# Optimization experiments

Hardware: AMD Instinct MI355X
Metric: run time of the kernel (lower is better)

## Reference

```python
import jax, jax.numpy as jnp
import numpy as np

D_MODEL = 1024
NUM_HEADS = 16
HEAD_DIM = D_MODEL // NUM_HEADS
B, S = 4, 2048


def setup_inputs() -> dict:
    key = jax.random.key(0)
    ks = jax.random.split(key, 11)
    scale = 1.0 / np.sqrt(D_MODEL)
    return {
        "query": jax.random.normal(ks[0], (B, S, D_MODEL), dtype=jnp.float32),
        "key": jax.random.normal(ks[1], (B, S, D_MODEL), dtype=jnp.float32),
        "value": jax.random.normal(ks[2], (B, S, D_MODEL), dtype=jnp.float32),
        "Wq": jax.random.normal(ks[3], (D_MODEL, D_MODEL), dtype=jnp.float32) * scale,
        "bq": jnp.zeros((D_MODEL,), dtype=jnp.float32),
        "Wk": jax.random.normal(ks[4], (D_MODEL, D_MODEL), dtype=jnp.float32) * scale,
        "bk": jnp.zeros((D_MODEL,), dtype=jnp.float32),
        "Wv": jax.random.normal(ks[5], (D_MODEL, D_MODEL), dtype=jnp.float32) * scale,
        "bv": jnp.zeros((D_MODEL,), dtype=jnp.float32),
        "Wo": jax.random.normal(ks[6], (D_MODEL, D_MODEL), dtype=jnp.float32) * scale,
        "bo": jnp.zeros((D_MODEL,), dtype=jnp.float32),
    }


def reference(query, key, value, Wq, bq, Wk, bk, Wv, bv, Wo, bo):
    b = query.shape[0]
    # QKV projections, split into heads: [B, H, S, hd]
    Q = (query @ Wq + bq).reshape(b, -1, NUM_HEADS, HEAD_DIM).transpose(0, 2, 1, 3)
    K = (key @ Wk + bk).reshape(b, -1, NUM_HEADS, HEAD_DIM).transpose(0, 2, 1, 3)
    V = (value @ Wv + bv).reshape(b, -1, NUM_HEADS, HEAD_DIM).transpose(0, 2, 1, 3)
    # scaled dot-product attention, full [B, H, S, S] scores (as in original)
    scores = jnp.einsum("bhqd,bhkd->bhqk", Q, K) / jnp.sqrt(
        jnp.asarray(HEAD_DIM, dtype=jnp.float32))
    attn = jax.nn.softmax(scores, axis=-1)
    out = jnp.einsum("bhqk,bhkd->bhqd", attn, V)
    out = out.transpose(0, 2, 1, 3).reshape(b, -1, D_MODEL)
    return out @ Wo + bo
```

## Files before the change

kernel.cpp:

```cpp
#include <hip/hip_runtime.h>
#include <hip/hip_bf16.h>

typedef _Float16 f16;
typedef _Float16 f16x8 __attribute__((ext_vector_type(8)));
typedef _Float16 f16x4 __attribute__((ext_vector_type(4)));
typedef __fp16 h16x2 __attribute__((ext_vector_type(2)));
typedef float f32x4 __attribute__((ext_vector_type(4)));

#define D_MODEL 1024
#define NHEAD 16
#define HD 64
#define BATCH 4
#define SEQ 2048
#define TOK (BATCH * SEQ)

__device__ __forceinline__ void gload_lds16(const void* g, void* l) {
  __builtin_amdgcn_global_load_lds(
      (const __attribute__((address_space(1))) unsigned int*)g,
      (__attribute__((address_space(3))) unsigned int*)l, 16, 0, 0);
}

__device__ __forceinline__ f16x8 fragF16_64(const char* rowptr, int g, int c) {
  union { uint4 u; f16x8 v; } r;
  r.u = *reinterpret_cast<const uint4*>(rowptr + ((g * 16) ^ ((c & 3) << 4)));
  return r.v;
}
__device__ __forceinline__ f16x8 fragF32_128(const char* rowptr, int g, int c) {
  const int s = (c & 7) << 4;
  union { uint4 u; float f[4]; } a, b;
  a.u = *reinterpret_cast<const uint4*>(rowptr + ((g * 32) ^ s));
  b.u = *reinterpret_cast<const uint4*>(rowptr + ((g * 32 + 16) ^ s));
  f16x8 r;
  r[0] = (f16)a.f[0]; r[1] = (f16)a.f[1]; r[2] = (f16)a.f[2]; r[3] = (f16)a.f[3];
  r[4] = (f16)b.f[0]; r[5] = (f16)b.f[1]; r[6] = (f16)b.f[2]; r[7] = (f16)b.f[3];
  return r;
}
__device__ __forceinline__ f16x8 lds_frag(const char* rowptr, int cb0, int s) {
  const uint2 a = *reinterpret_cast<const uint2*>(rowptr + (cb0 ^ s));
  const uint2 b = *reinterpret_cast<const uint2*>(rowptr + ((cb0 + 32) ^ s));
  union { unsigned int u[4]; f16x8 v; } r;
  r.u[0] = a.x; r.u[1] = a.y; r.u[2] = b.x; r.u[3] = b.y;
  return r.v;
}

__global__ __launch_bounds__(256) void transpose_cvt4_k(
    const float* __restrict__ w0, const float* __restrict__ w1,
    const float* __restrict__ w2, const float* __restrict__ w3,
    f16* __restrict__ t0, f16* __restrict__ t1, f16* __restrict__ t2,
    f16* __restrict__ t3) {
  __shared__ float tile[32][33];
  const float* W = blockIdx.z == 0 ? w0 : blockIdx.z == 1 ? w1 : blockIdx.z == 2 ? w2 : w3;
  f16* Wt = blockIdx.z == 0 ? t0 : blockIdx.z == 1 ? t1 : blockIdx.z == 2 ? t2 : t3;
  int n0 = blockIdx.x * 32, k0 = blockIdx.y * 32;
  int tx = threadIdx.x & 31, ty = threadIdx.x >> 5;
#pragma unroll
  for (int i = 0; i < 32; i += 8)
    tile[ty + i][tx] = W[(size_t)(k0 + ty + i) * D_MODEL + n0 + tx];
  __syncthreads();
#pragma unroll
  for (int i = 0; i < 32; i += 8)
    Wt[(size_t)(n0 + ty + i) * D_MODEL + k0 + tx] = (f16)tile[tx][ty + i];
}

template <bool A_F32, bool B_F32, bool OUT_F32, bool BIAS_ROW, bool SWZ>
__global__ __launch_bounds__(512) void gemm_k(
    const void* __restrict__ Ap, const void* __restrict__ Bp,
    const float* __restrict__ bias, void* __restrict__ Cout,
    int M, int N, int K, float scale) {
  constexpr int ABUF = A_F32 ? 16384 : 8192;
  constexpr int BBUF = B_F32 ? 16384 : 8192;
  constexpr int BUF = ABUF + BBUF;
  constexpr int NA = A_F32 ? 2 : 1;
  constexpr int NB = B_F32 ? 2 : 1;
  __shared__ char smem[2 * BUF];
  const int tid = threadIdx.x;
  const int lane = tid & 63, wid = tid >> 6;
  const int g = lane >> 4, c = lane & 15;
  const int wm = wid >> 1, wn = wid & 1;
  int btx, bty;
  if constexpr (SWZ) {
    int lin = blockIdx.x + blockIdx.y * 8;
    int xcd = lin & 7, rest = lin >> 3;
    bty = xcd * 8 + (rest & 7);
    btx = rest >> 3;
  } else {
    btx = blockIdx.x; bty = blockIdx.y;
  }
  const size_t brow = (size_t)bty * 128, bcol = (size_t)btx * 128;

  f32x4 acc[2][4];
#pragma unroll
  for (int i = 0; i < 2; ++i)
#pragma unroll
    for (int j = 0; j < 4; ++j) acc[i][j] = (f32x4){0.f, 0.f, 0.f, 0.f};

  const char* ga[NA];
  const char* gb[NB];
#pragma unroll
  for (int j = 0; j < NA; ++j) {
    int ch = wid * NA + j;
    if constexpr (A_F32) {
      int row = ch * 8 + (lane >> 3);
      ga[j] = (const char*)Ap + ((size_t)(brow + row) * K) * 4 +
              (((lane & 7) * 16) ^ ((row & 7) << 4));
    } else {
      int row = ch * 16 + (lane >> 2);
      ga[j] = (const char*)Ap + ((size_t)(brow + row) * K) * 2 +
              (((lane & 3) * 16) ^ ((row & 3) << 4));
    }
  }
#pragma unroll
  for (int j = 0; j < NB; ++j) {
    int ch = wid * NB + j;
    if constexpr (B_F32) {
      int row = ch * 8 + (lane >> 3);
      gb[j] = (const char*)Bp + ((size_t)(bcol + row) * K) * 4 +
              (((lane & 7) * 16) ^ ((row & 7) << 4));
    } else {
      int row = ch * 16 + (lane >> 2);
      gb[j] = (const char*)Bp + ((size_t)(bcol + row) * K) * 2 +
              (((lane & 3) * 16) ^ ((row & 3) << 4));
    }
  }
  auto stage = [&](char* buf) {
#pragma unroll
    for (int j = 0; j < NA; ++j) {
      gload_lds16(ga[j], buf + (wid * NA + j) * 1024);
      ga[j] += A_F32 ? 128 : 64;
    }
#pragma unroll
    for (int j = 0; j < NB; ++j) {
      gload_lds16(gb[j], buf + ABUF + (wid * NB + j) * 1024);
      gb[j] += B_F32 ? 128 : 64;
    }
  };

  stage(smem);
  const int nt = K / 32;
  for (int t = 0; t < nt; ++t) {
    char* cur = smem + (size_t)(t & 1) * BUF;
    char* nxt = smem + (size_t)((t + 1) & 1) * BUF;
    asm volatile("s_waitcnt vmcnt(0)" ::: "memory");
    __syncthreads();
    if (t + 1 < nt) stage(nxt);

    f16x8 Af[2], Bf[4];
#pragma unroll
    for (int fm = 0; fm < 2; ++fm) {
      int row = wm * 32 + fm * 16 + c;
      if constexpr (A_F32) Af[fm] = fragF32_128(cur + row * 128, g, c);
      else Af[fm] = fragF16_64(cur + row * 64, g, c);
    }
#pragma unroll
    for (int fn = 0; fn < 4; ++fn) {
      int row = wn * 64 + fn * 16 + c;
      if constexpr (B_F32) Bf[fn] = fragF32_128(cur + ABUF + row * 128, g, c);
      else Bf[fn] = fragF16_64(cur + ABUF + row * 64, g, c);
    }
#pragma unroll
    for (int fm = 0; fm < 2; ++fm)
#pragma unroll
      for (int fn = 0; fn < 4; ++fn)
        acc[fm][fn] = __builtin_amdgcn_mfma_f32_16x16x32_f16(Af[fm], Bf[fn],
                                                             acc[fm][fn], 0, 0, 0);
  }

#pragma unroll
  for (int fn = 0; fn < 4; ++fn) {
    size_t col = bcol + wn * 64 + fn * 16 + c;
    float cbias = BIAS_ROW ? 0.f : bias[col];
#pragma unroll
    for (int fm = 0; fm < 2; ++fm) {
#pragma unroll
      for (int r = 0; r < 4; ++r) {
        size_t row = brow + wm * 32 + fm * 16 + g * 4 + r;
        float v = (acc[fm][fn][r] + (BIAS_ROW ? bias[row] : cbias)) * scale;
        if (OUT_F32)
          ((float*)Cout)[row * (size_t)N + col] = v;
        else
          ((f16*)Cout)[row * (size_t)N + col] = (f16)v;
      }
    }
  }
}

__global__ __launch_bounds__(512) void attn_k(const f16* __restrict__ Q,
                                              const f16* __restrict__ Kp,
                                              const f16* __restrict__ Vt,
                                              f16* __restrict__ AO) {
  __shared__ char smem[65536];
  const int tid = threadIdx.x, lane = tid & 63, wid = tid >> 6;
  const int g = lane >> 4, c = lane & 15;
  const int b = blockIdx.x >> 4, h = blockIdx.x & 15;
  const int qt = blockIdx.y;
  const size_t qrow0 = (size_t)b * SEQ + (size_t)qt * 256;
  const int sr = lane >> 3;
  const int sc = (lane & 7) * 16;
  const float NEG_M = -8.65617025f;
  constexpr int NT = SEQ / 64;

#pragma unroll
  for (int j = 0; j < 4; ++j) {
    int ch = wid * 4 + j;
    int row = ch * 8 + sr;
    const char* gq = (const char*)Q + ((qrow0 + row) * D_MODEL + h * HD) * 2 +
                     (sc ^ (sr << 4));
    gload_lds16(gq, smem + ch * 1024);
  }
  asm volatile("s_waitcnt vmcnt(0)" ::: "memory");
  __syncthreads();

  f16x8 Qf[2][2];
#pragma unroll
  for (int fq = 0; fq < 2; ++fq) {
    int row = wid * 32 + fq * 16 + c;
#pragma unroll
    for (int kk = 0; kk < 2; ++kk) {
      union { uint4 u; f16x8 v; } r;
      r.u = *reinterpret_cast<const uint4*>(
          smem + row * 128 + ((kk * 64 + g * 16) ^ ((c & 7) << 4)));
      Qf[fq][kk] = r.v;
    }
  }
  __syncthreads();

  const char* gk;
  const char* gv;
  {
    int row = wid * 8 + sr;
    gk = (const char*)Kp + (((size_t)b * SEQ + row) * D_MODEL + h * HD) * 2 +
         (sc ^ (sr << 4));
    gv = (const char*)Vt + ((size_t)(h * HD + row) * TOK + (size_t)b * SEQ) * 2 +
         (sc ^ (sr << 4));
  }
#pragma unroll
  for (int tt = 0; tt < 3; ++tt) {
    gload_lds16(gk, smem + tt * 8192 + wid * 1024);
    gload_lds16(gv, smem + 32768 + tt * 8192 + wid * 1024);
    gk += (size_t)64 * D_MODEL * 2;
    gv += 64 * 2;
  }

  f16x8 ones_f;
#pragma unroll
  for (int j = 0; j < 8; ++j) ones_f[j] = (c == 0) ? (f16)1.0f : (f16)0.0f;

  f32x4 o[4][2];
#pragma unroll
  for (int i = 0; i < 4; ++i)
#pragma unroll
    for (int j = 0; j < 2; ++j) o[i][j] = (f32x4){0.f, 0.f, 0.f, 0.f};
  f32x4 o_l[2] = {(f32x4){0.f, 0.f, 0.f, 0.f}, (f32x4){0.f, 0.f, 0.f, 0.f}};

  for (int t = 0; t < NT; ++t) {
    if (t < NT - 2)
      asm volatile("s_waitcnt vmcnt(4)" ::: "memory");
    else if (t == NT - 2)
      asm volatile("s_waitcnt vmcnt(2)" ::: "memory");
    else
      asm volatile("s_waitcnt vmcnt(0)" ::: "memory");
    __builtin_amdgcn_s_barrier();
    asm volatile("" ::: "memory");
    if (t + 3 < NT) {
      gload_lds16(gk, smem + ((t + 3) & 3) * 8192 + wid * 1024);
      gload_lds16(gv, smem + 32768 + ((t + 3) & 3) * 8192 + wid * 1024);
      gk += (size_t)64 * D_MODEL * 2;
      gv += 64 * 2;
    }
    const char* Ks = smem + (t & 3) * 8192;
    const char* Vs = smem + 32768 + (t & 3) * 8192;

    f32x4 st[4][2];
#pragma unroll
    for (int i = 0; i < 4; ++i)
#pragma unroll
      for (int j = 0; j < 2; ++j)
        st[i][j] = (f32x4){NEG_M, NEG_M, NEG_M, NEG_M};
#pragma unroll
    for (int kk = 0; kk < 2; ++kk) {
      f16x8 Kf[4];
#pragma unroll
      for (int km = 0; km < 4; ++km) {
        int row = km * 16 + c;
        union { uint4 u; f16x8 v; } r;
        r.u = *reinterpret_cast<const uint4*>(
            Ks + row * 128 + ((kk * 64 + g * 16) ^ ((c & 7) << 4)));
        Kf[km] = r.v;
      }
      __builtin_amdgcn_s_setprio(1);
#pragma unroll
      for (int km = 0; km < 4; ++km)
#pragma unroll
        for (int fq = 0; fq < 2; ++fq)
          st[km][fq] = __builtin_amdgcn_mfma_f32_16x16x32_f16(Kf[km], Qf[fq][kk],
                                                              st[km][fq], 0, 0, 0);
      __builtin_amdgcn_s_setprio(0);
    }

    f16x8 pb[2][2];
#pragma unroll
    for (int fq = 0; fq < 2; ++fq) {
#pragma unroll
      for (int km = 0; km < 4; ++km)
#pragma unroll
        for (int r = 0; r < 4; ++r)
          st[km][fq][r] = __builtin_amdgcn_exp2f(st[km][fq][r]);
#pragma unroll
      for (int k2 = 0; k2 < 2; ++k2) {
        union { h16x2 h2[4]; f16x8 v; } u;
        u.h2[0] = __builtin_amdgcn_cvt_pkrtz(st[2 * k2][fq][0], st[2 * k2][fq][1]);
        u.h2[1] = __builtin_amdgcn_cvt_pkrtz(st[2 * k2][fq][2], st[2 * k2][fq][3]);
        u.h2[2] = __builtin_amdgcn_cvt_pkrtz(st[2 * k2 + 1][fq][0], st[2 * k2 + 1][fq][1]);
        u.h2[3] = __builtin_amdgcn_cvt_pkrtz(st[2 * k2 + 1][fq][2], st[2 * k2 + 1][fq][3]);
        pb[k2][fq] = u.v;
      }
    }

#pragma unroll
    for (int k2 = 0; k2 < 2; ++k2) {
      f16x8 Vf[4];
#pragma unroll
      for (int fhd = 0; fhd < 4; ++fhd) {
        int row = fhd * 16 + c;
        Vf[fhd] = lds_frag(Vs + row * 128, k2 * 64 + g * 8, (row & 7) << 4);
      }
      __builtin_amdgcn_s_setprio(1);
#pragma unroll
      for (int fhd = 0; fhd < 4; ++fhd)
#pragma unroll
        for (int fq = 0; fq < 2; ++fq)
          o[fhd][fq] = __builtin_amdgcn_mfma_f32_16x16x32_f16(Vf[fhd], pb[k2][fq],
                                                              o[fhd][fq], 0, 0, 0);
#pragma unroll
      for (int fq = 0; fq < 2; ++fq)
        o_l[fq] = __builtin_amdgcn_mfma_f32_16x16x32_f16(ones_f, pb[k2][fq],
                                                         o_l[fq], 0, 0, 0);
      __builtin_amdgcn_s_setprio(0);
    }
  }

#pragma unroll
  for (int fq = 0; fq < 2; ++fq) {
    float L = __shfl(o_l[fq][0], c);
    float rl = 1.0f / L;
    size_t token = qrow0 + wid * 32 + fq * 16 + c;
#pragma unroll
    for (int fhd = 0; fhd < 4; ++fhd) {
      f16x4 vv;
#pragma unroll
      for (int r = 0; r < 4; ++r) vv[r] = (f16)(o[fhd][fq][r] * rl);
      *reinterpret_cast<f16x4*>(AO + token * D_MODEL + h * HD + fhd * 16 + g * 4) = vv;
    }
  }
}

extern "C" void kernel_launch(void* const* d_in, const int* in_sizes, int n_in,
                              void* d_out, int out_size, void* d_ws, size_t ws_size,
                              hipStream_t stream) {
  const float* q32 = (const float*)d_in[0];
  const float* k32 = (const float*)d_in[1];
  const float* v32 = (const float*)d_in[2];
  const float* Wq = (const float*)d_in[3];
  const float* bq = (const float*)d_in[4];
  const float* Wk = (const float*)d_in[5];
  const float* bk = (const float*)d_in[6];
  const float* Wv = (const float*)d_in[7];
  const float* bv = (const float*)d_in[8];
  const float* Wo = (const float*)d_in[9];
  const float* bo = (const float*)d_in[10];

  const size_t TOKD = (size_t)TOK * D_MODEL;
  const size_t WD = (size_t)D_MODEL * D_MODEL;
  f16* Qp = (f16*)d_ws;
  f16* Kp = Qp + TOKD;
  f16* Vt = Kp + TOKD;
  f16* AO = Vt + TOKD;
  f16* Wqt = AO + TOKD;
  f16* Wkt = Wqt + WD;
  f16* Wvt = Wkt + WD;
  f16* Wot = Wvt + WD;

  dim3 tg(32, 32, 4);
  transpose_cvt4_k<<<tg, 256, 0, stream>>>(Wq, Wk, Wv, Wo, Wqt, Wkt, Wvt, Wot);

  dim3 gq(D_MODEL / 128, TOK / 128);
  gemm_k<true, false, false, false, true><<<gq, 512, 0, stream>>>(
      q32, Wqt, bq, Qp, TOK, D_MODEL, D_MODEL, 0.18033688f);
  gemm_k<true, false, false, false, true><<<gq, 512, 0, stream>>>(
      k32, Wkt, bk, Kp, TOK, D_MODEL, D_MODEL, 1.0f);
  dim3 gv(TOK / 128, D_MODEL / 128);
  gemm_k<false, true, false, true, false><<<gv, 512, 0, stream>>>(
      Wvt, v32, bv, Vt, D_MODEL, TOK, D_MODEL, 1.0f);

  dim3 ga(BATCH * NHEAD, SEQ / 256);
  attn_k<<<ga, 512, 0, stream>>>(Qp, Kp, Vt, AO);

  gemm_k<false, false, true, false, true><<<gq, 512, 0, stream>>>(
      AO, Wot, bo, (float*)d_out, TOK, D_MODEL, D_MODEL, 1.0f);
}
```

Measured before the change: 212.1 us.

## Use 4-wave GEMM blocks with larger per-wave tiles and merge Q/K projections

Each GEMM block now runs 256 threads (4 waves) instead of 8, and each wave computes a 64x64 output sub-tile (4x4 MFMA fragments) instead of 32x64. This doubles register-level reuse of the B fragments. Every thread now issues twice as many global-to-LDS loads per stage. The Q and K projection GEMMs are merged into one launch that uses blockIdx.z to select operands, which removes one launch and lets the two run together. Possible costs are higher register pressure, which can lower occupancy, and less latency hiding with fewer waves per block.

```diff
diff --git a/kernel.cpp b/kernel.cpp
--- a/kernel.cpp
+++ b/kernel.cpp
@@ -62,35 +62,26 @@
     Wt[(size_t)(n0 + ty + i) * D_MODEL + k0 + tx] = (f16)tile[tx][ty + i];
 }
 
-template <bool A_F32, bool B_F32, bool OUT_F32, bool BIAS_ROW, bool SWZ>
-__global__ __launch_bounds__(512) void gemm_k(
+template <bool A_F32, bool B_F32, bool OUT_F32, bool BIAS_ROW>
+__device__ __forceinline__ void gemm_body(
     const void* __restrict__ Ap, const void* __restrict__ Bp,
     const float* __restrict__ bias, void* __restrict__ Cout,
-    int M, int N, int K, float scale) {
+    int M, int N, int K, float scale, int btx, int bty) {
   constexpr int ABUF = A_F32 ? 16384 : 8192;
   constexpr int BBUF = B_F32 ? 16384 : 8192;
   constexpr int BUF = ABUF + BBUF;
-  constexpr int NA = A_F32 ? 2 : 1;
-  constexpr int NB = B_F32 ? 2 : 1;
+  constexpr int NA = A_F32 ? 4 : 2;
+  constexpr int NB = B_F32 ? 4 : 2;
   __shared__ char smem[2 * BUF];
   const int tid = threadIdx.x;
   const int lane = tid & 63, wid = tid >> 6;
   const int g = lane >> 4, c = lane & 15;
   const int wm = wid >> 1, wn = wid & 1;
-  int btx, bty;
-  if constexpr (SWZ) {
-    int lin = blockIdx.x + blockIdx.y * 8;
-    int xcd = lin & 7, rest = lin >> 3;
-    bty = xcd * 8 + (rest & 7);
-    btx = rest >> 3;
-  } else {
-    btx = blockIdx.x; bty = blockIdx.y;
-  }
   const size_t brow = (size_t)bty * 128, bcol = (size_t)btx * 128;
 
-  f32x4 acc[2][4];
-#pragma unroll
-  for (int i = 0; i < 2; ++i)
+  f32x4 acc[4][4];
+#pragma unroll
+  for (int i = 0; i < 4; ++i)
 #pragma unroll
     for (int j = 0; j < 4; ++j) acc[i][j] = (f32x4){0.f, 0.f, 0.f, 0.f};
 
@@ -144,10 +135,10 @@
     __syncthreads();
     if (t + 1 < nt) stage(nxt);
 
-    f16x8 Af[2], Bf[4];
-#pragma unroll
-    for (int fm = 0; fm < 2; ++fm) {
-      int row = wm * 32 + fm * 16 + c;
+    f16x8 Af[4], Bf[4];
+#pragma unroll
+    for (int fm = 0; fm < 4; ++fm) {
+      int row = wm * 64 + fm * 16 + c;
       if constexpr (A_F32) Af[fm] = fragF32_128(cur + row * 128, g, c);
       else Af[fm] = fragF16_64(cur + row * 64, g, c);
     }
@@ -158,7 +149,7 @@
       else Bf[fn] = fragF16_64(cur + ABUF + row * 64, g, c);
     }
 #pragma unroll
-    for (int fm = 0; fm < 2; ++fm)
+    for (int fm = 0; fm < 4; ++fm)
 #pragma unroll
       for (int fn = 0; fn < 4; ++fn)
         acc[fm][fn] = __builtin_amdgcn_mfma_f32_16x16x32_f16(Af[fm], Bf[fn],
@@ -170,10 +161,10 @@
     size_t col = bcol + wn * 64 + fn * 16 + c;
     float cbias = BIAS_ROW ? 0.f : bias[col];
 #pragma unroll
-    for (int fm = 0; fm < 2; ++fm) {
+    for (int fm = 0; fm < 4; ++fm) {
 #pragma unroll
       for (int r = 0; r < 4; ++r) {
-        size_t row = brow + wm * 32 + fm * 16 + g * 4 + r;
+        size_t row = brow + wm * 64 + fm * 16 + g * 4 + r;
         float v = (acc[fm][fn][r] + (BIAS_ROW ? bias[row] : cbias)) * scale;
         if (OUT_F32)
           ((float*)Cout)[row * (size_t)N + col] = v;
@@ -182,6 +173,41 @@
       }
     }
   }
+}
+
+__device__ __forceinline__ void swz_map(int& btx, int& bty) {
+  int lin = blockIdx.x + blockIdx.y * 8;
+  int xcd = lin & 7, rest = lin >> 3;
+  bty = xcd * 8 + (rest & 7);
+  btx = rest >> 3;
+}
+
+template <bool A_F32, bool B_F32, bool OUT_F32, bool BIAS_ROW, bool SWZ>
+__global__ __launch_bounds__(256) void gemm_k(
+    const void* __restrict__ Ap, const void* __restrict__ Bp,
+    const float* __restrict__ bias, void* __restrict__ Cout,
+    int M, int N, int K, float scale) {
+  int btx, bty;
+  if constexpr (SWZ) swz_map(btx, bty);
+  else { btx = blockIdx.x; bty = blockIdx.y; }
+  gemm_body<A_F32, B_F32, OUT_F32, BIAS_ROW>(Ap, Bp, bias, Cout, M, N, K, scale,
+                                             btx, bty);
+}
+
+__global__ __launch_bounds__(256) void qkproj_k(
+    const float* __restrict__ q32, const float* __restrict__ k32,
+    const f16* __restrict__ Wqt, const f16* __restrict__ Wkt,
+    const float* __restrict__ bq, const float* __restrict__ bk,
+    f16* __restrict__ Qp, f16* __restrict__ Kp, float qscale) {
+  int btx, bty;
+  swz_map(btx, bty);
+  const void* Ap = blockIdx.z ? (const void*)k32 : (const void*)q32;
+  const void* Bp = blockIdx.z ? (const void*)Wkt : (const void*)Wqt;
+  const float* bias = blockIdx.z ? bk : bq;
+  void* Cout = blockIdx.z ? (void*)Kp : (void*)Qp;
+  float scale = blockIdx.z ? 1.0f : qscale;
+  gemm_body<true, false, false, false>(Ap, Bp, bias, Cout, TOK, D_MODEL, D_MODEL,
+                                       scale, btx, bty);
 }
 
 __global__ __launch_bounds__(512) void attn_k(const f16* __restrict__ Q,
@@ -383,18 +409,17 @@
   dim3 tg(32, 32, 4);
   transpose_cvt4_k<<<tg, 256, 0, stream>>>(Wq, Wk, Wv, Wo, Wqt, Wkt, Wvt, Wot);
 
-  dim3 gq(D_MODEL / 128, TOK / 128);
-  gemm_k<true, false, false, false, true><<<gq, 512, 0, stream>>>(
-      q32, Wqt, bq, Qp, TOK, D_MODEL, D_MODEL, 0.18033688f);
-  gemm_k<true, false, false, false, true><<<gq, 512, 0, stream>>>(
-      k32, Wkt, bk, Kp, TOK, D_MODEL, D_MODEL, 1.0f);
+  dim3 gqk(8, 64, 2);
+  qkproj_k<<<gqk, 256, 0, stream>>>(q32, k32, Wqt, Wkt, bq, bk, Qp, Kp,
+                                    0.18033688f);
   dim3 gv(TOK / 128, D_MODEL / 128);
-  gemm_k<false, true, false, true, false><<<gv, 512, 0, stream>>>(
+  gemm_k<false, true, false, true, false><<<gv, 256, 0, stream>>>(
       Wvt, v32, bv, Vt, D_MODEL, TOK, D_MODEL, 1.0f);
 
   dim3 ga(BATCH * NHEAD, SEQ / 256);
   attn_k<<<ga, 512, 0, stream>>>(Qp, Kp, Vt, AO);
 
-  gemm_k<false, false, true, false, true><<<gq, 512, 0, stream>>>(
+  dim3 gq(D_MODEL / 128, TOK / 128);
+  gemm_k<false, false, true, false, true><<<gq, 256, 0, stream>>>(
       AO, Wot, bo, (float*)d_out, TOK, D_MODEL, D_MODEL, 1.0f);
 }
```

Measured after the change: 194.2 us. 1.09x faster.
